# Performance work log

Hardware: AMD Instinct MI355X
Metric: run time of the kernel (lower is better)

## Reference

```python
import jax, jax.numpy as jnp
import numpy as np
from jax import lax

VOCAB, D_EMB, D_HID, N_CLS = 32000, 512, 512, 4
B, T = 32, 2048


def setup_inputs() -> dict:
    key = jax.random.key(0)
    ks = jax.random.split(key, 8)
    s_emb = 1.0 / np.sqrt(D_EMB)
    s_hid = 1.0 / np.sqrt(D_HID)
    return {
        "x": jax.random.randint(ks[0], (B, T), 0, VOCAB, dtype=jnp.int64),
        "attn": jnp.ones((B, T), dtype=jnp.int32),
        "embedding": jax.random.normal(ks[1], (VOCAB, D_EMB), jnp.float32) * s_emb,
        "W_ih": jax.random.uniform(ks[2], (4 * D_HID, D_EMB), jnp.float32, -s_hid, s_hid),
        "W_hh": jax.random.uniform(ks[3], (4 * D_HID, D_HID), jnp.float32, -s_hid, s_hid),
        "b_ih": jax.random.uniform(ks[4], (4 * D_HID,), jnp.float32, -s_hid, s_hid),
        "b_hh": jax.random.uniform(ks[5], (4 * D_HID,), jnp.float32, -s_hid, s_hid),
        "fc_W": jax.random.uniform(ks[6], (N_CLS, D_HID), jnp.float32, -s_hid, s_hid),
        "fc_b": jax.random.uniform(ks[7], (N_CLS,), jnp.float32, -s_hid, s_hid),
    }


def _lstm_forward(x, embedding, W_ih, W_hh, b_ih, b_hh):
    b, t = x.shape
    h_dim = W_hh.shape[1]
    emb = embedding[x]                                  # [B, T, E]
    # input projection for all timesteps at once (same math as per-step cell)
    x_proj = jnp.einsum('bte,ge->tbg', emb, W_ih) + b_ih  # [T, B, 4H]

    def step(carry, xp):
        h, c = carry
        gates = xp + h @ W_hh.T + b_hh                  # [B, 4H]
        i, f, g, o = jnp.split(gates, 4, axis=-1)
        c = jax.nn.sigmoid(f) * c + jax.nn.sigmoid(i) * jnp.tanh(g)
        h = jax.nn.sigmoid(o) * jnp.tanh(c)
        return (h, c), h

    h0 = jnp.zeros((b, h_dim), emb.dtype)
    (_, _), hs = lax.scan(step, (h0, h0), x_proj)       # hs: [T, B, H]
    return hs


def reference(x, attn, embedding, W_ih, W_hh, b_ih, b_hh, fc_W, fc_b):
    hs = _lstm_forward(x, embedding, W_ih, W_hh, b_ih, b_hh)  # [T, B, H]
    lengths = jnp.sum(attn, axis=1).astype(jnp.int32) - 1     # [B]
    last_hs = hs[lengths, jnp.arange(hs.shape[1])]            # [B, H] vectorized gather
    logits = last_hs @ fc_W.T + fc_b                          # [B, n_classes]
    return logits
```

## Files before the change

kernel.cpp:

```cpp
#include <hip/hip_runtime.h>
#include <math.h>

typedef unsigned int u32;

#define T_SEQ   2048
#define NWG     256

#define OFF_HBUF   0
#define OFF_CNT    131072
#define OFF_LASTH  133120
#define WS_NEED    198656ull

#define FB_OFF_HBUF   0
#define FB_OFF_ARRIVE 131072
#define FB_OFF_LASTH  131328

#define DYN_LDS_BYTES 148480

__device__ __forceinline__ float sigm(float x) { return 1.0f / (1.0f + expf(-x)); }

__device__ __forceinline__ float4 ldg4s(const float* p) {
  float4 v;
  asm volatile("global_load_dwordx4 %0, %1, off sc0 sc1" : "=v"(v) : "v"(p) : "memory");
  return v;
}
__device__ __forceinline__ void stg1fs(float* p, float v) {
  asm volatile("global_store_dword %0, %1, off sc0 sc1" :: "v"(p), "v"(v) : "memory");
}

__global__ void __launch_bounds__(256, 1)
lstm_seq(const int* __restrict__ x, const int* __restrict__ attn,
         const float* __restrict__ emb,
         const float* __restrict__ Wih, const float* __restrict__ Whh,
         const float* __restrict__ bih, const float* __restrict__ bhh,
         float* __restrict__ hbuf, u32* __restrict__ counters,
         float* __restrict__ lasth)
{
  extern __shared__ __align__(16) char smem[];
  float4* Wl4 = (float4*)smem;
  float4* Hl4 = (float4*)(smem + 131072);
  float*  gsc = (float*)(smem + 131072 + 16384);
  __shared__ int s_dead;

  const int tid = threadIdx.x, bid = blockIdx.x;
  const int ug = bid >> 2, bg = bid & 3;
  const int wv = tid >> 6, lane = tid & 63;
  const int kg = lane >> 2, inner = lane & 3;
  const int rowg = wv * 2 + (inner >> 1);
  const int bbase = (inner & 1) * 4;

  u32* cnt = counters + bg * 64;

#pragma unroll
  for (int k = 0; k < 32; ++k) {
    int cf = tid + k * 256;
    int r  = cf >> 8, c = cf & 255;
    int R  = (r >> 3) * 512 + ug * 8 + (r & 7);
    const float* src = (c < 128) ? (Wih + (size_t)R * 512 + c * 4)
                                 : (Whh + (size_t)R * 512 + (c - 128) * 4);
    float4 v = *(const float4*)src;
    int p = r * 256 + (c & ~7) + (((c & 7) + ((c >> 3) & 15) + (r >> 2)) & 7);
    Wl4[p] = v;
  }

  {
    int b = tid & 7, c = tid >> 3;
    const int4* ap = (const int4*)(attn + (size_t)(bg * 8 + b) * 2048 + c * 64);
    int s = 0;
#pragma unroll
    for (int k = 0; k < 16; ++k) { int4 a = ap[k]; s += a.x + a.y + a.z + a.w; }
    gsc[c * 8 + b] = (float)s;
  }
  if (tid == 0) s_dead = 0;
  __syncthreads();
  int len = 0; float c_reg = 0.f;
  float bI = 0, bF = 0, bG = 0, bO = 0;
  if (tid < 64) {
    int b = tid & 7, uu = tid >> 3;
    int s = 0;
#pragma unroll
    for (int c = 0; c < 32; ++c) s += (int)gsc[c * 8 + b];
    len = s - 1; if (len < 0) len = T_SEQ - 1;
    int gu = ug * 8 + uu;
    bI = bih[gu]        + bhh[gu];
    bF = bih[512 + gu]  + bhh[512 + gu];
    bG = bih[1024 + gu] + bhh[1024 + gu];
    bO = bih[1536 + gu] + bhh[1536 + gu];
  }
  __syncthreads();

  bool dead = false;
  float4 w[4][8];

  for (int t = 0; t < T_SEQ; ++t) {
    float acc[4][4];
#pragma unroll
    for (int i = 0; i < 4; ++i) { acc[i][0] = 0.f; acc[i][1] = 0.f; acc[i][2] = 0.f; acc[i][3] = 0.f; }

#pragma unroll
    for (int i = 0; i < 4; ++i) {
      int r = rowg * 4 + i;
#pragma unroll
      for (int q = 0; q < 8; ++q)
        w[i][q] = Wl4[r * 256 + kg * 8 + ((q + kg + rowg) & 7)];
    }
#pragma unroll
    for (int jb = 0; jb < 4; ++jb) {
      int xr = x[(size_t)(bg * 8 + bbase + jb) * 2048 + t];
      const float4* ep = (const float4*)(emb + (size_t)xr * 512 + kg * 32);
      float4 e[8];
#pragma unroll
      for (int q = 0; q < 8; ++q) e[q] = ep[q];
#pragma unroll
      for (int q = 0; q < 8; ++q)
#pragma unroll
        for (int i = 0; i < 4; ++i) {
          acc[i][jb] += w[i][q].x * e[q].x; acc[i][jb] += w[i][q].y * e[q].y;
          acc[i][jb] += w[i][q].z * e[q].z; acc[i][jb] += w[i][q].w * e[q].w;
        }
    }

    if (tid == 0 && !dead) {
      int it = 0;
      const u32 target = (u32)(t << 6);
      while (__hip_atomic_load(cnt, __ATOMIC_RELAXED, __HIP_MEMORY_SCOPE_AGENT) < target) {
        if (++it > (1 << 16)) { s_dead = 1; break; }
        __builtin_amdgcn_s_sleep(4);
      }
    }
    __syncthreads();
    if (s_dead) dead = true;

    {
      const float* hsrc = hbuf + (((t + 1) & 1) << 14) + (size_t)(bg * 8) * 512;
      float4 hv[4];
      int pp[4];
#pragma unroll
      for (int k = 0; k < 4; ++k) {
        int cf = tid + k * 256;
        int b = cf >> 7, c = cf & 127;
        hv[k] = ldg4s(hsrc + (size_t)b * 512 + c * 4);
        pp[k] = b * 128 + (c & ~7) + (((c & 7) + (c >> 3) + b) & 7);
      }
      asm volatile("s_waitcnt vmcnt(0)" ::: "memory");
      __builtin_amdgcn_sched_barrier(0);
#pragma unroll
      for (int k = 0; k < 4; ++k) Hl4[pp[k]] = hv[k];
    }
    __syncthreads();

#pragma unroll
    for (int i = 0; i < 4; ++i) {
      int r = rowg * 4 + i;
#pragma unroll
      for (int q = 0; q < 8; ++q)
        w[i][q] = Wl4[r * 256 + 128 + kg * 8 + ((q + kg + rowg) & 7)];
    }
#pragma unroll
    for (int jb = 0; jb < 4; ++jb) {
      int bl = bbase + jb;
      float4 e[8];
#pragma unroll
      for (int q = 0; q < 8; ++q)
        e[q] = Hl4[bl * 128 + kg * 8 + ((q + kg + bl) & 7)];
#pragma unroll
      for (int q = 0; q < 8; ++q)
#pragma unroll
        for (int i = 0; i < 4; ++i) {
          acc[i][jb] += w[i][q].x * e[q].x; acc[i][jb] += w[i][q].y * e[q].y;
          acc[i][jb] += w[i][q].z * e[q].z; acc[i][jb] += w[i][q].w * e[q].w;
        }
    }

#pragma unroll
    for (int i = 0; i < 4; ++i)
#pragma unroll
      for (int j = 0; j < 4; ++j) {
        float v = acc[i][j];
        v += __shfl_xor(v, 4, 64);
        v += __shfl_xor(v, 8, 64);
        v += __shfl_xor(v, 16, 64);
        v += __shfl_xor(v, 32, 64);
        acc[i][j] = v;
      }
    if (lane < 16) {
      int kgl = lane >> 2;
      int r = rowg * 4 + kgl;
#pragma unroll
      for (int j = 0; j < 4; ++j)
        gsc[r * 8 + bbase + j] = acc[kgl][j];
    }
    __syncthreads();

    if (tid < 64) {
      int b = tid & 7, uu = tid >> 3;
      float gi = gsc[(0 * 8 + uu) * 8 + b] + bI;
      float gf = gsc[(1 * 8 + uu) * 8 + b] + bF;
      float gg = gsc[(2 * 8 + uu) * 8 + b] + bG;
      float go = gsc[(3 * 8 + uu) * 8 + b] + bO;
      float iv = sigm(gi), fv = sigm(gf), ov = sigm(go), gv = tanhf(gg);
      c_reg = fv * c_reg + iv * gv;
      float hval = ov * tanhf(c_reg);
      int bglob = bg * 8 + b, unit = ug * 8 + uu;
      float* hd = hbuf + ((t & 1) << 14) + (bglob << 9) + unit;
      stg1fs(hd, hval);
      if (t == len) lasth[(bglob << 9) + unit] = hval;
      asm volatile("s_waitcnt vmcnt(0)" ::: "memory");
      if (tid == 0)
        __hip_atomic_fetch_add(cnt, 1u, __ATOMIC_RELAXED, __HIP_MEMORY_SCOPE_AGENT);
    }
  }
}

__global__ void __launch_bounds__(128)
fc_kernel(const float* __restrict__ lasth, const float* __restrict__ fcW,
          const float* __restrict__ fcb, float* __restrict__ out)
{
  int tid = threadIdx.x;
  int b = tid >> 2, n = tid & 3;
  const float4* h4 = (const float4*)(lasth + (size_t)b * 512);
  const float4* w4 = (const float4*)(fcW + (size_t)n * 512);
  float s0 = 0.f, s1 = 0.f, s2 = 0.f, s3 = 0.f;
#pragma unroll 8
  for (int k = 0; k < 128; ++k) {
    float4 a = h4[k], c = w4[k];
    s0 += a.x * c.x; s1 += a.y * c.y; s2 += a.z * c.z; s3 += a.w * c.w;
  }
  out[b * 4 + n] = fcb[n] + ((s0 + s1) + (s2 + s3));
}

__device__ __forceinline__ void gl2lds16(const void* gsrc, void* ldst) {
  __builtin_amdgcn_global_load_lds(
      (const __attribute__((address_space(1))) u32*)gsrc,
      (__attribute__((address_space(3))) u32*)ldst, 16, 0, 0);
}

__global__ void __launch_bounds__(256)
lstm_persist(const int* __restrict__ xidx, const int* __restrict__ attn,
             const float* __restrict__ emb,
             const float* __restrict__ Wih, const float* __restrict__ Whh,
             const float* __restrict__ bih, const float* __restrict__ bhh,
             float* __restrict__ hbuf, float* __restrict__ lasth,
             u32* __restrict__ arrive)
{
  __shared__ __align__(16) float Wl[8][1024];
  __shared__ __align__(16) float ul[2][32][64];
  __shared__ float gsc[32][8];

  const int tid  = threadIdx.x;
  const int wg   = blockIdx.x;
  const int lane = tid & 63;
  const int wv   = tid >> 6;
  const int r    = tid & 7;
  const int bb   = tid >> 3;
  const int brl  = bb & 7;

#pragma unroll 2
  for (int i = 0; i < 8; ++i) {
    int ci = i * 256 + tid;
    int rr = ci >> 8;
    int cc = ci & 255;
    int R  = ((rr >> 1) << 9) + (wg * 2 + (rr & 1));
    const float* src = (cc < 128) ? (Wih + (size_t)R * 512 + cc * 4)
                                  : (Whh + (size_t)R * 512 + (cc - 128) * 4);
    float4 v = *(const float4*)src;
    int slot = cc ^ (rr & 7);
    *(float4*)&Wl[rr][slot * 4] = v;
  }
  float bias;
  {
    int R = ((r >> 1) << 9) + (wg * 2 + (r & 1));
    bias = bih[R] + bhh[R];
  }
  {
    int pb = tid >> 3, pc = tid & 7;
    const int4* ap = (const int4*)(attn + pb * 2048 + pc * 256);
    int s = 0;
#pragma unroll 8
    for (int k = 0; k < 64; ++k) { int4 a = ap[k]; s += a.x + a.y + a.z + a.w; }
    gsc[pb][pc] = (float)s;
  }
  __syncthreads();
  int   len_reg = 0;
  float c_reg   = 0.f;
  if (tid < 64) {
    int b2 = tid & 31;
    int s = 0;
#pragma unroll
    for (int k = 0; k < 8; ++k) s += (int)gsc[b2][k];
    len_reg = s - 1;
    if (len_reg < 0) len_reg = 2047;
  }
  __syncthreads();

  const int idx_b = 8 * wv + (lane & 7);
  int idx_cur = xidx[(size_t)idx_b * 2048];

  for (int t = 0; t < T_SEQ; ++t) {
    int idx_next = (t < T_SEQ - 1) ? xidx[(size_t)idx_b * 2048 + t + 1] : 0;
    float a0 = bias, a1 = 0.f, a2 = 0.f, a3 = 0.f;
    const float* hsrc = hbuf + (((t + 1) & 1) << 14);

    auto stageE = [&](int jt, int buf) {
#pragma unroll
      for (int q = 0; q < 2; ++q) {
        int rlq = 4 * q + (lane >> 4);
        int sc = lane & 15;
        int kc = sc ^ (rlq & 7);
        int rowg = __shfl(idx_cur, rlq, 64);
        const float* g = emb + (size_t)rowg * 512 + jt * 64 + kc * 4;
        gl2lds16(g, (void*)&ul[buf][8 * wv + 4 * q][0]);
      }
    };
    auto stageH = [&](int jt, int buf) {
#pragma unroll
      for (int q = 0; q < 2; ++q) {
        int rlq = 4 * q + (lane >> 4);
        int sc = lane & 15;
        int kc = sc ^ (rlq & 7);
        int blq = 8 * wv + rlq;
        const float* g = hsrc + (size_t)blq * 512 + jt * 64 + kc * 4;
        gl2lds16(g, (void*)&ul[buf][8 * wv + 4 * q][0]);
      }
    };
    auto computeT = [&](int jg, int buf) {
#pragma unroll
      for (int kc = 0; kc < 16; ++kc) {
        float4 uv4 = *(const float4*)&ul[buf][bb][(kc ^ brl) * 4];
        float4 wv4 = *(const float4*)&Wl[r][(((jg << 4) + kc) ^ r) * 4];
        a0 += uv4.x * wv4.x; a1 += uv4.y * wv4.y;
        a2 += uv4.z * wv4.z; a3 += uv4.w * wv4.w;
      }
    };

    stageE(0, 0);
#pragma unroll
    for (int jt = 0; jt < 8; ++jt) {
      if (jt < 7) { stageE(jt + 1, (jt + 1) & 1); asm volatile("s_waitcnt vmcnt(2)" ::: "memory"); }
      else       { asm volatile("s_waitcnt vmcnt(0)" ::: "memory"); }
      computeT(jt, jt & 1);
    }

    if (tid == 0) {
      u32 target = (u32)t << 8;
      while (__hip_atomic_load(arrive, __ATOMIC_RELAXED, __HIP_MEMORY_SCOPE_AGENT) < target)
        __builtin_amdgcn_s_sleep(2);
    }
    __syncthreads();
    __builtin_amdgcn_fence(__ATOMIC_ACQUIRE, "agent");

    stageH(0, 0);
#pragma unroll
    for (int jt = 0; jt < 8; ++jt) {
      if (jt < 7) { stageH(jt + 1, (jt + 1) & 1); asm volatile("s_waitcnt vmcnt(2)" ::: "memory"); }
      else       { asm volatile("s_waitcnt vmcnt(0)" ::: "memory"); }
      computeT(8 + jt, jt & 1);
    }

    gsc[bb][r] = a0 + a1 + a2 + a3;
    __syncthreads();
    if (tid < 64) {
      int u  = tid >> 5;
      int b2 = tid & 31;
      float gi = gsc[b2][u];
      float gf = gsc[b2][2 + u];
      float gg = gsc[b2][4 + u];
      float go = gsc[b2][6 + u];
      float iv = sigm(gi), fv = sigm(gf), ov = sigm(go);
      float gv = tanhf(gg);
      c_reg = fv * c_reg + iv * gv;
      float hv = ov * tanhf(c_reg);
      int unit = (wg << 1) + u;
      hbuf[((t & 1) << 14) + (b2 << 9) + unit] = hv;
      if (t == len_reg) lasth[(b2 << 9) + unit] = hv;
      __builtin_amdgcn_fence(__ATOMIC_RELEASE, "agent");
      if (tid == 0)
        __hip_atomic_fetch_add(arrive, 1u, __ATOMIC_RELAXED, __HIP_MEMORY_SCOPE_AGENT);
    }
    idx_cur = idx_next;
  }
}

extern "C" void kernel_launch(void* const* d_in, const int* in_sizes, int n_in,
                              void* d_out, int out_size, void* d_ws, size_t ws_size,
                              hipStream_t stream) {
  const int*   x    = (const int*)d_in[0];
  const int*   attn = (const int*)d_in[1];
  const float* emb  = (const float*)d_in[2];
  const float* Wih  = (const float*)d_in[3];
  const float* Whh  = (const float*)d_in[4];
  const float* bih  = (const float*)d_in[5];
  const float* bhh  = (const float*)d_in[6];
  const float* fcW  = (const float*)d_in[7];
  const float* fcb  = (const float*)d_in[8];
  float* out = (float*)d_out;
  char* ws = (char*)d_ws;

  if (ws_size >= WS_NEED) {
    float* hbuf  = (float*)(ws + OFF_HBUF);
    u32*   cnts  = (u32*)(ws + OFF_CNT);
    float* lasth = (float*)(ws + OFF_LASTH);

    (void)hipFuncSetAttribute((const void*)lstm_seq,
                              hipFuncAttributeMaxDynamicSharedMemorySize, DYN_LDS_BYTES);
    (void)hipMemsetAsync(ws, 0, 133120, stream);

    hipLaunchKernelGGL(lstm_seq, dim3(NWG), dim3(256), DYN_LDS_BYTES, stream,
                       x, attn, emb, Wih, Whh, bih, bhh, hbuf, cnts, lasth);
    hipLaunchKernelGGL(fc_kernel, dim3(1), dim3(128), 0, stream,
                       lasth, fcW, fcb, out);
  } else {
    float* hbuf   = (float*)(ws + FB_OFF_HBUF);
    u32*   arrive = (u32*)(ws + FB_OFF_ARRIVE);
    float* lasth  = (float*)(ws + FB_OFF_LASTH);
    (void)hipMemsetAsync(ws, 0, 131072 + 256, stream);
    hipLaunchKernelGGL(lstm_persist, dim3(256), dim3(256), 0, stream,
                       x, attn, emb, Wih, Whh, bih, bhh, hbuf, lasth, arrive);
    hipLaunchKernelGGL(fc_kernel, dim3(1), dim3(128), 0, stream,
                       lasth, fcW, fcb, out);
  }
}
```

Before: 13.60 ms.

## Double LSTM workgroup size to 512 threads, halving per-thread gate rows

The persistent LSTM kernel now runs 512 threads per workgroup instead of 256. Each wave handles two gate rows and four batch columns, so per-thread work and register pressure are halved and more waves are available to hide LDS and global latency within the serial timestep loop. The weight-staging, attention-sum and h-broadcast loops are re-strided to match, and the attention partial sums now go to scratch in the H buffer region. The cost is more threads taking part in each per-step barrier and reduction.

After: 13.70 ms. No clear change (+0.7%).

```diff
diff --git a/kernel.cpp b/kernel.cpp
--- a/kernel.cpp
+++ b/kernel.cpp
@@ -28,7 +28,7 @@
   asm volatile("global_store_dword %0, %1, off sc0 sc1" :: "v"(p), "v"(v) : "memory");
 }
 
-__global__ void __launch_bounds__(256, 1)
+__global__ void __launch_bounds__(512, 1)
 lstm_seq(const int* __restrict__ x, const int* __restrict__ attn,
          const float* __restrict__ emb,
          const float* __restrict__ Wih, const float* __restrict__ Whh,
@@ -45,15 +45,16 @@
   const int tid = threadIdx.x, bid = blockIdx.x;
   const int ug = bid >> 2, bg = bid & 3;
   const int wv = tid >> 6, lane = tid & 63;
-  const int kg = lane >> 2, inner = lane & 3;
-  const int rowg = wv * 2 + (inner >> 1);
-  const int bbase = (inner & 1) * 4;
+  const int rgrp = wv >> 1;
+  const int bh   = wv & 1;
+  const int kg   = lane >> 2;
+  const int inner = lane & 3;
 
   u32* cnt = counters + bg * 64;
 
 #pragma unroll
-  for (int k = 0; k < 32; ++k) {
-    int cf = tid + k * 256;
+  for (int k = 0; k < 16; ++k) {
+    int cf = tid + k * 512;
     int r  = cf >> 8, c = cf & 255;
     int R  = (r >> 3) * 512 + ug * 8 + (r & 7);
     const float* src = (c < 128) ? (Wih + (size_t)R * 512 + c * 4)
@@ -64,22 +65,24 @@
   }
 
   {
+    float* scratch = (float*)Hl4;
     int b = tid & 7, c = tid >> 3;
-    const int4* ap = (const int4*)(attn + (size_t)(bg * 8 + b) * 2048 + c * 64);
+    const int4* ap = (const int4*)(attn + (size_t)(bg * 8 + b) * 2048 + c * 32);
     int s = 0;
 #pragma unroll
-    for (int k = 0; k < 16; ++k) { int4 a = ap[k]; s += a.x + a.y + a.z + a.w; }
-    gsc[c * 8 + b] = (float)s;
+    for (int k = 0; k < 8; ++k) { int4 a = ap[k]; s += a.x + a.y + a.z + a.w; }
+    scratch[c * 8 + b] = (float)s;
   }
   if (tid == 0) s_dead = 0;
   __syncthreads();
   int len = 0; float c_reg = 0.f;
   float bI = 0, bF = 0, bG = 0, bO = 0;
   if (tid < 64) {
+    const float* scratch = (const float*)Hl4;
     int b = tid & 7, uu = tid >> 3;
     int s = 0;
 #pragma unroll
-    for (int c = 0; c < 32; ++c) s += (int)gsc[c * 8 + b];
+    for (int c = 0; c < 64; ++c) s += (int)scratch[c * 8 + b];
     len = s - 1; if (len < 0) len = T_SEQ - 1;
     int gu = ug * 8 + uu;
     bI = bih[gu]        + bhh[gu];
@@ -90,31 +93,35 @@
   __syncthreads();
 
   bool dead = false;
-  float4 w[4][8];
 
   for (int t = 0; t < T_SEQ; ++t) {
-    float acc[4][4];
-#pragma unroll
-    for (int i = 0; i < 4; ++i) { acc[i][0] = 0.f; acc[i][1] = 0.f; acc[i][2] = 0.f; acc[i][3] = 0.f; }
-
-#pragma unroll
-    for (int i = 0; i < 4; ++i) {
-      int r = rowg * 4 + i;
+    float acc[2][4];
+#pragma unroll
+    for (int i = 0; i < 2; ++i) { acc[i][0] = 0.f; acc[i][1] = 0.f; acc[i][2] = 0.f; acc[i][3] = 0.f; }
+
+    float4 w[2][8];
+#pragma unroll
+    for (int i = 0; i < 2; ++i) {
+      int r = rgrp * 8 + inner + 4 * i;
 #pragma unroll
       for (int q = 0; q < 8; ++q)
-        w[i][q] = Wl4[r * 256 + kg * 8 + ((q + kg + rowg) & 7)];
-    }
+        w[i][q] = Wl4[r * 256 + kg * 8 + ((q + kg + (r >> 2)) & 7)];
+    }
+
+    int xr[4];
+#pragma unroll
+    for (int jb = 0; jb < 4; ++jb)
+      xr[jb] = x[(size_t)(bg * 8 + bh * 4 + jb) * 2048 + t];
 #pragma unroll
     for (int jb = 0; jb < 4; ++jb) {
-      int xr = x[(size_t)(bg * 8 + bbase + jb) * 2048 + t];
-      const float4* ep = (const float4*)(emb + (size_t)xr * 512 + kg * 32);
+      const float4* ep = (const float4*)(emb + (size_t)xr[jb] * 512 + kg * 32);
       float4 e[8];
 #pragma unroll
       for (int q = 0; q < 8; ++q) e[q] = ep[q];
 #pragma unroll
       for (int q = 0; q < 8; ++q)
 #pragma unroll
-        for (int i = 0; i < 4; ++i) {
+        for (int i = 0; i < 2; ++i) {
           acc[i][jb] += w[i][q].x * e[q].x; acc[i][jb] += w[i][q].y * e[q].y;
           acc[i][jb] += w[i][q].z * e[q].z; acc[i][jb] += w[i][q].w * e[q].w;
         }
@@ -133,11 +140,11 @@
 
     {
       const float* hsrc = hbuf + (((t + 1) & 1) << 14) + (size_t)(bg * 8) * 512;
-      float4 hv[4];
-      int pp[4];
-#pragma unroll
-      for (int k = 0; k < 4; ++k) {
-        int cf = tid + k * 256;
+      float4 hv[2];
+      int pp[2];
+#pragma unroll
+      for (int k = 0; k < 2; ++k) {
+        int cf = tid + k * 512;
         int b = cf >> 7, c = cf & 127;
         hv[k] = ldg4s(hsrc + (size_t)b * 512 + c * 4);
         pp[k] = b * 128 + (c & ~7) + (((c & 7) + (c >> 3) + b) & 7);
@@ -145,20 +152,21 @@
       asm volatile("s_waitcnt vmcnt(0)" ::: "memory");
       __builtin_amdgcn_sched_barrier(0);
 #pragma unroll
-      for (int k = 0; k < 4; ++k) Hl4[pp[k]] = hv[k];
+      for (int k = 0; k < 2; ++k) Hl4[pp[k]] = hv[k];
     }
     __syncthreads();
 
 #pragma unroll
-    for (int i = 0; i < 4; ++i) {
-      int r = rowg * 4 + i;
+    for (int i = 0; i < 2; ++i) {
+      int r = rgrp * 8 + inner + 4 * i;
 #pragma unroll
       for (int q = 0; q < 8; ++q)
-        w[i][q] = Wl4[r * 256 + 128 + kg * 8 + ((q + kg + rowg) & 7)];
-    }
+        w[i][q] = Wl4[r * 256 + 128 + kg * 8 + ((q + kg + (r >> 2)) & 7)];
+    }
+
 #pragma unroll
     for (int jb = 0; jb < 4; ++jb) {
-      int bl = bbase + jb;
+      int bl = bh * 4 + jb;
       float4 e[8];
 #pragma unroll
       for (int q = 0; q < 8; ++q)
@@ -166,38 +174,40 @@
 #pragma unroll
       for (int q = 0; q < 8; ++q)
 #pragma unroll
-        for (int i = 0; i < 4; ++i) {
+        for (int i = 0; i < 2; ++i) {
           acc[i][jb] += w[i][q].x * e[q].x; acc[i][jb] += w[i][q].y * e[q].y;
           acc[i][jb] += w[i][q].z * e[q].z; acc[i][jb] += w[i][q].w * e[q].w;
         }
     }
 
 #pragma unroll
-    for (int i = 0; i < 4; ++i)
-#pragma unroll
-      for (int j = 0; j < 4; ++j) {
-        float v = acc[i][j];
+    for (int i = 0; i < 2; ++i)
+#pragma unroll
+      for (int jb = 0; jb < 4; ++jb) {
+        float v = acc[i][jb];
         v += __shfl_xor(v, 4, 64);
         v += __shfl_xor(v, 8, 64);
         v += __shfl_xor(v, 16, 64);
         v += __shfl_xor(v, 32, 64);
-        acc[i][j] = v;
-      }
-    if (lane < 16) {
-      int kgl = lane >> 2;
-      int r = rowg * 4 + kgl;
-#pragma unroll
-      for (int j = 0; j < 4; ++j)
-        gsc[r * 8 + bbase + j] = acc[kgl][j];
+        acc[i][jb] = v;
+      }
+    if (kg == 0) {
+#pragma unroll
+      for (int i = 0; i < 2; ++i) {
+        int r = rgrp * 8 + inner + 4 * i;
+#pragma unroll
+        for (int jb = 0; jb < 4; ++jb)
+          gsc[r * 8 + bh * 4 + jb] = acc[i][jb];
+      }
     }
     __syncthreads();
 
     if (tid < 64) {
       int b = tid & 7, uu = tid >> 3;
-      float gi = gsc[(0 * 8 + uu) * 8 + b] + bI;
-      float gf = gsc[(1 * 8 + uu) * 8 + b] + bF;
-      float gg = gsc[(2 * 8 + uu) * 8 + b] + bG;
-      float go = gsc[(3 * 8 + uu) * 8 + b] + bO;
+      float gi = gsc[(0  + uu) * 8 + b] + bI;
+      float gf = gsc[(8  + uu) * 8 + b] + bF;
+      float gg = gsc[(16 + uu) * 8 + b] + bG;
+      float go = gsc[(24 + uu) * 8 + b] + bO;
       float iv = sigm(gi), fv = sigm(gf), ov = sigm(go), gv = tanhf(gg);
       c_reg = fv * c_reg + iv * gv;
       float hval = ov * tanhf(c_reg);
@@ -403,9 +413,9 @@
 
     (void)hipFuncSetAttribute((const void*)lstm_seq,
                               hipFuncAttributeMaxDynamicSharedMemorySize, DYN_LDS_BYTES);
-    (void)hipMemsetAsync(ws, 0, 133120, stream);
-
-    hipLaunchKernelGGL(lstm_seq, dim3(NWG), dim3(256), DYN_LDS_BYTES, stream,
+    (void)hipMemsetAsync(ws, 0, OFF_LASTH, stream);
+
+    hipLaunchKernelGGL(lstm_seq, dim3(NWG), dim3(512), DYN_LDS_BYTES, stream,
                        x, attn, emb, Wih, Whh, bih, bhh, hbuf, cnts, lasth);
     hipLaunchKernelGGL(fc_kernel, dim3(1), dim3(128), 0, stream,
                        lasth, fcW, fcb, out);
```
